# Kernel tuning notes

Measured on AMD Instinct MI355X. Metric: run time of the kernel, lower is better.

The kernel has to match this reference:

```python
import jax, jax.numpy as jnp
import numpy as np

NEG_SLOPE = 0.01  # nn.LeakyReLU default
N_NODES = 38332
POI_LEN = 38333
CAT_LEN = 400
POI_DIM = 300
CAT_DIM = 100
GCN_CH = 64
GCN_LAYERS = 5
N_EDGES = N_NODES * 32


def leaky(x):
    return jnp.where(x >= 0, x, NEG_SLOPE * x)


def gcn_conv(x, src, dst, W, b):
    """PyG GCNConv: add self loops + symmetric normalization.
    out = D^-1/2 (A+I) D^-1/2 X W + b, deg computed with self loops."""
    n = x.shape[0]
    h = x @ W  # [N, out]
    deg = jax.ops.segment_sum(jnp.ones_like(dst, dtype=h.dtype), dst, num_segments=n) + 1.0
    dinv = jax.lax.rsqrt(deg)  # deg >= 1 always (self loop)
    norm = dinv[src] * dinv[dst]  # [E]
    agg = jax.ops.segment_sum(h[src] * norm[:, None], dst, num_segments=n)
    agg = agg + h * (1.0 / deg)[:, None]  # self-loop term: norm_ii = 1/deg_i
    return agg + b


def setup_inputs() -> dict:
    key = jax.random.key(0)
    ks = jax.random.split(key, 16)
    poi_ids = jax.random.randint(ks[0], (N_NODES, 1), 0, POI_LEN).astype(jnp.float32)
    cat_ids = jax.random.randint(ks[1], (N_NODES, 1), 0, CAT_LEN).astype(jnp.float32)
    feats = jax.random.normal(ks[2], (N_NODES, 3), dtype=jnp.float32)
    x = jnp.concatenate([poi_ids, cat_ids, feats], axis=1)  # [N,5]
    edge_index = jax.random.randint(ks[3], (2, N_EDGES), 0, N_NODES, dtype=jnp.int32)

    def glorot(k, shape):
        lim = float(np.sqrt(6.0 / (shape[0] + shape[1])))
        return jax.random.uniform(k, shape, jnp.float32, -lim, lim)

    d_in = POI_DIM + CAT_DIM + 3  # 403
    params = {
        "poi_emb": jax.random.normal(ks[4], (POI_LEN, POI_DIM), jnp.float32),
        "cat_emb": jax.random.normal(ks[5], (CAT_LEN, CAT_DIM), jnp.float32),
        "W_in": glorot(ks[6], (d_in, GCN_CH)),
        "b_in": jnp.zeros((GCN_CH,), jnp.float32),
        "gcn_Ws": jnp.stack([glorot(jax.random.fold_in(ks[7], i), (GCN_CH, GCN_CH)) for i in range(GCN_LAYERS)]),
        "gcn_bs": jnp.zeros((GCN_LAYERS, GCN_CH), jnp.float32),
        "W_out": glorot(ks[8], (GCN_CH, 1)),
        "b_out": jnp.zeros((1,), jnp.float32),
        "fc1_W": glorot(ks[9], (N_NODES, 128)),
        "fc1_b": jnp.zeros((128,), jnp.float32),
        "fc2_W": glorot(ks[10], (128, POI_LEN)),
        "fc2_b": jnpos if False else jnp.zeros((POI_LEN,), jnp.float32),
    }
    return {"x": x, "edge_index": edge_index, **params}


def reference(x, edge_index, poi_emb, cat_emb, W_in, b_in, gcn_Ws, gcn_bs, W_out, b_out, fc1_W, fc1_b, fc2_W, fc2_b):
    src, dst = edge_index[0], edge_index[1]
    poi_f = poi_emb[x[:, 0].astype(jnp.int32)]  # [N,300]
    cat_f = cat_emb[x[:, 1].astype(jnp.int32)]  # [N,100]
    feat = jnp.concatenate([poi_f, cat_f, x[:, 2:5]], axis=1)  # [N,403]
    feat = leaky(gcn_conv(feat, src, dst, W_in, b_in))
    for i in range(GCN_LAYERS):
        t = gcn_conv(feat, src, dst, gcn_Ws[i], gcn_bs[i])
        feat = leaky(t) + t  # GcnUnit: relu(temp) + temp
    feat = leaky(gcn_conv(feat, src, dst, W_out, b_out)).reshape(-1)  # [N]
    h = jax.nn.relu(feat @ fc1_W + fc1_b)
    out = jax.nn.relu(h @ fc2_W + fc2_b)  # [poi_len]
    return out
```

## Files before the change

kernel.cpp:

```cpp
#include <hip/hip_runtime.h>
#include <hip/hip_bf16.h>

#define N_NODES 38332
#define POI_LEN 38333
#define CAT_LEN 400
#define POI_DIM 300
#define CAT_DIM 100
#define N_EDGES (N_NODES * 32)
#define NEG_SLOPE 0.01f
#define B1 ((N_NODES + 127) / 128)
#define SPLIT_CHUNK 2048
#define NSPLIT ((N_EDGES + SPLIT_CHUNK - 1) / SPLIT_CHUNK)
#define PLACE_CAP 8192
#define BCAP 8192

typedef __attribute__((ext_vector_type(8))) short short8;
typedef __attribute__((ext_vector_type(4))) float f32x4;

__device__ __forceinline__ unsigned short f2bf(float f) {
  unsigned u = __float_as_uint(f);
  u += 0x7fff + ((u >> 16) & 1);
  return (unsigned short)(u >> 16);
}
__device__ __forceinline__ float bflo(unsigned u) {
  return __uint_as_float(u << 16);
}
__device__ __forceinline__ float bfhi(unsigned u) {
  return __uint_as_float(u & 0xffff0000u);
}


#define WFIN_ELEMS (13 * 2048)
#define WFGCN_ELEMS (5 * 4096)

__global__ __launch_bounds__(256) void k_prep(const float* __restrict__ W_in,
                                              const float* __restrict__ gcn_Ws,
                                              unsigned short* __restrict__ wf_in,
                                              unsigned short* __restrict__ wf_gcn,
                                              int* __restrict__ bcnt,
                                              float* __restrict__ h128) {
  int idx = blockIdx.x * 256 + threadIdx.x;
  if (idx < B1) bcnt[idx] = 0;
  if (idx < 128) h128[idx] = 0.f;
  if (idx < WFIN_ELEMS) {
    int j = idx & 7, n = (idx >> 3) & 63, q = (idx >> 9) & 3, ks = idx >> 11;
    int k = ks * 32 + q * 8 + j;
    wf_in[idx] = f2bf((k < 400) ? W_in[k * 64 + n] : 0.f);
  } else if (idx < WFIN_ELEMS + WFGCN_ELEMS) {
    int t = idx - WFIN_ELEMS;
    int l = t >> 12, i = t & 4095;
    int j = i & 7, n = (i >> 3) & 63, q = (i >> 9) & 3, ks = i >> 11;
    int k = ks * 32 + q * 8 + j;
    wf_gcn[t] = f2bf(gcn_Ws[(size_t)l * 4096 + k * 64 + n]);
  }
}


__global__ __launch_bounds__(256) void k_split(const int* __restrict__ src,
                                               const int* __restrict__ dst,
                                               int* __restrict__ bcnt,
                                               int* __restrict__ staging) {
  __shared__ int hist[B1];
  __shared__ int lbase[B1];
  __shared__ int lcur[B1];
  int tid = threadIdx.x;
  int base = blockIdx.x * SPLIT_CHUNK;
  int n = N_EDGES - base;
  if (n > SPLIT_CHUNK) n = SPLIT_CHUNK;
  for (int b = tid; b < B1; b += 256) {
    hist[b] = 0;
    lcur[b] = 0;
  }
  __syncthreads();
  for (int i = tid; i < n; i += 256) atomicAdd(&hist[dst[base + i] >> 7], 1);
  __syncthreads();
  for (int b = tid; b < B1; b += 256) {
    int c = hist[b];
    lbase[b] = c ? atomicAdd(&bcnt[b], c) : 0;
  }
  __syncthreads();
  for (int i = tid; i < n; i += 256) {
    int d = dst[base + i];
    int s = src[base + i];
    int b = d >> 7;
    int off = atomicAdd(&lcur[b], 1);
    staging[(size_t)b * BCAP + lbase[b] + off] = (s << 7) | (d & 127);
  }
}

__global__ __launch_bounds__(256) void k_place(const int* __restrict__ staging,
                                               const int* __restrict__ bcnt,
                                               int* __restrict__ csr_src,
                                               int2* __restrict__ rs,
                                               float* __restrict__ dinv) {
  __shared__ int lc[128];
  __shared__ int ls[256];
  __shared__ int cur[128];
  __shared__ int buf[PLACE_CAP];
  int b = blockIdx.x;
  int tid = threadIdx.x;
  int d0 = b * 128;
  int nd = N_NODES - d0;
  if (nd > 128) nd = 128;
  int cnt_b = bcnt[b];
  const int* st = staging + (size_t)b * BCAP;
  if (tid < 128) lc[tid] = 0;
  __syncthreads();
  for (int i = tid; i < cnt_b; i += 256) atomicAdd(&lc[st[i] & 127], 1);
  __syncthreads();
  int v = (tid < 128) ? lc[tid] : 0;
  ls[tid] = v;
  __syncthreads();
  for (int off = 1; off < 128; off <<= 1) {
    int t = (tid >= off) ? ls[tid - off] : 0;
    __syncthreads();
    ls[tid] += t;
    __syncthreads();
  }
  if (tid < 128) {
    int excl = ls[tid] - v;
    cur[tid] = excl;
    if (tid < nd) {
      rs[d0 + tid] = make_int2(b * BCAP + excl, v);
      dinv[d0 + tid] = 1.0f / sqrtf((float)(v + 1));
    }
  }
  __syncthreads();
  for (int i = tid; i < cnt_b; i += 256) {
    int p = st[i];
    int pos = atomicAdd(&cur[p & 127], 1);
    buf[pos] = p >> 7;
  }
  __syncthreads();
  int base = b * BCAP;
  for (int i = tid; i < cnt_b; i += 256) csr_src[base + i] = buf[i];
}


__global__ __launch_bounds__(256) void k_front(
    const float* __restrict__ x, const float* __restrict__ poi_emb,
    const float* __restrict__ cat_emb, const float* __restrict__ W_in,
    const unsigned short* __restrict__ wf_in, const float* __restrict__ dinv,
    unsigned short* __restrict__ hs) {
  constexpr int KP = 416, RS = 424, NK4 = 104;
  __shared__ unsigned short sA[16 * RS];
  __shared__ float sC[16 * 68];
  __shared__ int sPid[16], sCid[16];
  __shared__ float sX[16][3];
  int tid = threadIdx.x;
  int row0 = blockIdx.x * 16;
  if (tid < 16) {
    int row = row0 + tid;
    if (row < N_NODES) {
      sPid[tid] = (int)x[row * 5 + 0];
      sCid[tid] = (int)x[row * 5 + 1];
      sX[tid][0] = x[row * 5 + 2];
      sX[tid][1] = x[row * 5 + 3];
      sX[tid][2] = x[row * 5 + 4];
    } else {
      sPid[tid] = 0; sCid[tid] = 0;
      sX[tid][0] = sX[tid][1] = sX[tid][2] = 0.f;
    }
  }
  __syncthreads();
  for (int idx = tid; idx < 16 * NK4; idx += 256) {
    int r = idx / NK4;
    int k = (idx - r * NK4) * 4;
    ushort4 o = {0, 0, 0, 0};
    if (k < 400 && row0 + r < N_NODES) {
      float4 f;
      if (k < 300) f = *(const float4*)(poi_emb + (size_t)sPid[r] * 300 + k);
      else         f = *(const float4*)(cat_emb + (size_t)sCid[r] * 100 + (k - 300));
      o.x = f2bf(f.x); o.y = f2bf(f.y); o.z = f2bf(f.z); o.w = f2bf(f.w);
    }
    *(ushort4*)&sA[r * RS + k] = o;
  }
  __syncthreads();
  int lane = tid & 63, wv = tid >> 6;
  int c = lane & 15, q = lane >> 4, n0 = wv * 16;
  f32x4 acc = {0.f, 0.f, 0.f, 0.f};
  const unsigned short* arow = &sA[c * RS];
#pragma unroll
  for (int ks = 0; ks < KP / 32; ks++) {
    short8 af = *(const short8*)(arow + ks * 32 + q * 8);
    short8 bf = *(const short8*)(wf_in + ((size_t)((ks * 4 + q) * 64 + n0 + c)) * 8);
    acc = __builtin_amdgcn_mfma_f32_16x16x32_bf16(af, bf, acc, 0, 0, 0);
  }
#pragma unroll
  for (int r = 0; r < 4; r++) sC[(q * 4 + r) * 68 + n0 + c] = acc[r];
  __syncthreads();
  for (int idx = tid; idx < 16 * 64; idx += 256) {
    int r = idx >> 6, col = idx & 63;
    int row = row0 + r;
    if (row < N_NODES) {
      float v = sC[r * 68 + col] + sX[r][0] * W_in[400 * 64 + col] +
                sX[r][1] * W_in[401 * 64 + col] + sX[r][2] * W_in[402 * 64 + col];
      hs[(size_t)row * 64 + col] = f2bf(v * dinv[row]);
    }
  }
}


template <int MODE>
__global__ __launch_bounds__(256) void k_agg(const unsigned short* __restrict__ hs,
                                             const int2* __restrict__ rs,
                                             const int* __restrict__ csr_src,
                                             const float* __restrict__ dinv,
                                             const float* __restrict__ bias,
                                             const unsigned short* __restrict__ Wf,
                                             unsigned short* __restrict__ hs_next,
                                             const float* __restrict__ W_out,
                                             float* __restrict__ hs1) {
  __shared__ unsigned short sA[16 * 72];
  __shared__ float sC[4 * 68];
  int tid = threadIdx.x;
  int lane = tid & 63;
  int wv = tid >> 6;
  int node = blockIdx.x * 4 + wv;
  int eslot = lane >> 3;
  int ch8 = lane & 7;
  if (MODE != 2) {
    for (int i = tid; i < 216; i += 256)
      *(ushort4*)&sA[288 + i * 4] = (ushort4){0, 0, 0, 0};
  }
  int2 rr = rs[node];
  int r0 = rr.x, r1 = rr.x + rr.y;
  float4 a0 = {0.f, 0.f, 0.f, 0.f}, a1 = a0;
#define ACC8(v)                                                              \
  do {                                                                       \
    a0.x += bflo((v).x); a0.y += bfhi((v).x);                                \
    a0.z += bflo((v).y); a0.w += bfhi((v).y);                                \
    a1.x += bflo((v).z); a1.y += bfhi((v).z);                                \
    a1.z += bflo((v).w); a1.w += bfhi((v).w);                                \
  } while (0)
  int e = r0 + eslot;
  for (; e + 24 < r1; e += 32) {
    int s0 = csr_src[e];
    int s1 = csr_src[e + 8];
    int s2 = csr_src[e + 16];
    int s3 = csr_src[e + 24];
    uint4 v0 = *(const uint4*)(hs + (size_t)s0 * 64 + ch8 * 8);
    uint4 v1 = *(const uint4*)(hs + (size_t)s1 * 64 + ch8 * 8);
    uint4 v2 = *(const uint4*)(hs + (size_t)s2 * 64 + ch8 * 8);
    uint4 v3 = *(const uint4*)(hs + (size_t)s3 * 64 + ch8 * 8);
    ACC8(v0); ACC8(v1); ACC8(v2); ACC8(v3);
  }
  if (e + 8 < r1) {
    int s0 = csr_src[e];
    int s1 = csr_src[e + 8];
    uint4 v0 = *(const uint4*)(hs + (size_t)s0 * 64 + ch8 * 8);
    uint4 v1 = *(const uint4*)(hs + (size_t)s1 * 64 + ch8 * 8);
    ACC8(v0); ACC8(v1);
    e += 16;
  }
  if (e < r1) {
    int s = csr_src[e];
    uint4 v = *(const uint4*)(hs + (size_t)s * 64 + ch8 * 8);
    ACC8(v);
  }
#undef ACC8
#pragma unroll
  for (int off = 8; off <= 32; off <<= 1) {
    a0.x += __shfl_xor(a0.x, off, 64);
    a0.y += __shfl_xor(a0.y, off, 64);
    a0.z += __shfl_xor(a0.z, off, 64);
    a0.w += __shfl_xor(a0.w, off, 64);
    a1.x += __shfl_xor(a1.x, off, 64);
    a1.y += __shfl_xor(a1.y, off, 64);
    a1.z += __shfl_xor(a1.z, off, 64);
    a1.w += __shfl_xor(a1.w, off, 64);
  }
  float dn = dinv[node];
  if (lane < 8) {
    uint4 sv = *(const uint4*)(hs + (size_t)node * 64 + ch8 * 8);
    float4 bb0 = *(const float4*)(bias + ch8 * 8);
    float4 bb1 = *(const float4*)(bias + ch8 * 8 + 4);
    float4 t0, t1;
    t0.x = dn * (a0.x + bflo(sv.x)) + bb0.x;
    t0.y = dn * (a0.y + bfhi(sv.x)) + bb0.y;
    t0.z = dn * (a0.z + bflo(sv.y)) + bb0.z;
    t0.w = dn * (a0.w + bfhi(sv.y)) + bb0.w;
    t1.x = dn * (a1.x + bflo(sv.z)) + bb1.x;
    t1.y = dn * (a1.y + bfhi(sv.z)) + bb1.y;
    t1.z = dn * (a1.z + bflo(sv.w)) + bb1.z;
    t1.w = dn * (a1.w + bfhi(sv.w)) + bb1.w;
    float4 l0, l1, o0, o1;
    l0.x = (t0.x >= 0.f) ? t0.x : NEG_SLOPE * t0.x;
    l0.y = (t0.y >= 0.f) ? t0.y : NEG_SLOPE * t0.y;
    l0.z = (t0.z >= 0.f) ? t0.z : NEG_SLOPE * t0.z;
    l0.w = (t0.w >= 0.f) ? t0.w : NEG_SLOPE * t0.w;
    l1.x = (t1.x >= 0.f) ? t1.x : NEG_SLOPE * t1.x;
    l1.y = (t1.y >= 0.f) ? t1.y : NEG_SLOPE * t1.y;
    l1.z = (t1.z >= 0.f) ? t1.z : NEG_SLOPE * t1.z;
    l1.w = (t1.w >= 0.f) ? t1.w : NEG_SLOPE * t1.w;
    if (MODE == 0) {
      o0 = l0; o1 = l1;
    } else {
      o0.x = l0.x + t0.x; o0.y = l0.y + t0.y; o0.z = l0.z + t0.z; o0.w = l0.w + t0.w;
      o1.x = l1.x + t1.x; o1.y = l1.y + t1.y; o1.z = l1.z + t1.z; o1.w = l1.w + t1.w;
    }
    if (MODE == 2) {
      float4 w0 = *(const float4*)(W_out + ch8 * 8);
      float4 w1 = *(const float4*)(W_out + ch8 * 8 + 4);
      float p = o0.x * w0.x + o0.y * w0.y + o0.z * w0.z + o0.w * w0.w +
                o1.x * w1.x + o1.y * w1.y + o1.z * w1.z + o1.w * w1.w;
      p += __shfl_xor(p, 1, 64);
      p += __shfl_xor(p, 2, 64);
      p += __shfl_xor(p, 4, 64);
      if (lane == 0) hs1[node] = p * dn;
    } else {
      uint4 pk;
      pk.x = (unsigned)f2bf(o0.x) | ((unsigned)f2bf(o0.y) << 16);
      pk.y = (unsigned)f2bf(o0.z) | ((unsigned)f2bf(o0.w) << 16);
      pk.z = (unsigned)f2bf(o1.x) | ((unsigned)f2bf(o1.y) << 16);
      pk.w = (unsigned)f2bf(o1.z) | ((unsigned)f2bf(o1.w) << 16);
      *(uint4*)&sA[wv * 72 + ch8 * 8] = pk;
    }
  }
  if (MODE != 2) {
    __syncthreads();
    int c = lane & 15, q = lane >> 4, n0 = wv * 16;
    f32x4 acc = {0.f, 0.f, 0.f, 0.f};
    const unsigned short* arow = &sA[c * 72];
#pragma unroll
    for (int ks = 0; ks < 2; ks++) {
      short8 af = *(const short8*)(arow + ks * 32 + q * 8);
      short8 bf = *(const short8*)(Wf + ((size_t)((ks * 4 + q) * 64 + n0 + c)) * 8);
      acc = __builtin_amdgcn_mfma_f32_16x16x32_bf16(af, bf, acc, 0, 0, 0);
    }
    if (q == 0) {
#pragma unroll
      for (int r = 0; r < 4; r++) sC[r * 68 + n0 + c] = acc[r];
    }
    __syncthreads();
    if (tid < 128) {
      int r = tid >> 5, c2 = (tid & 31) * 2;
      int row = blockIdx.x * 4 + r;
      float dr = dinv[row];
      unsigned lo = f2bf(sC[r * 68 + c2] * dr);
      unsigned hi = f2bf(sC[r * 68 + c2 + 1] * dr);
      *(unsigned*)(hs_next + (size_t)row * 64 + c2) = lo | (hi << 16);
    }
  }
}


__global__ __launch_bounds__(256) void k_out_agg(const float* __restrict__ hs1,
                                                 const int2* __restrict__ rs,
                                                 const int* __restrict__ csr_src,
                                                 const float* __restrict__ dinv,
                                                 const float* __restrict__ b_out,
                                                 float* __restrict__ g) {
  int lane = threadIdx.x & 63;
  int w = threadIdx.x >> 6;
  int node = blockIdx.x * 4 + w;
  int2 rr = rs[node];
  int r0 = rr.x, r1 = rr.x + rr.y;
  float acc = 0.f;
  for (int e = r0 + lane; e < r1; e += 64) acc += hs1[csr_src[e]];
#pragma unroll
  for (int off = 32; off; off >>= 1) acc += __shfl_xor(acc, off, 64);
  if (lane == 0) {
    float t = dinv[node] * (acc + hs1[node]) + b_out[0];
    g[node] = (t >= 0.f) ? t : NEG_SLOPE * t;
  }
}


__global__ __launch_bounds__(128) void k_fc1(const float* __restrict__ g,
                                             const float* __restrict__ fc1_W,
                                             float* __restrict__ h128) {
  int j = threadIdx.x;
  int base = blockIdx.x * 32;
  int end = base + 32;
  if (end > N_NODES) end = N_NODES;
  float acc = 0.f;
  int i = base;
  for (; i + 4 <= end; i += 4) {
    acc += g[i + 0] * fc1_W[(size_t)(i + 0) * 128 + j];
    acc += g[i + 1] * fc1_W[(size_t)(i + 1) * 128 + j];
    acc += g[i + 2] * fc1_W[(size_t)(i + 2) * 128 + j];
    acc += g[i + 3] * fc1_W[(size_t)(i + 3) * 128 + j];
  }
  for (; i < end; i++) acc += g[i] * fc1_W[(size_t)i * 128 + j];
  atomicAdd(&h128[j], acc);
}

__global__ __launch_bounds__(256) void k_fc2(const float* __restrict__ h128raw,
                                             const float* __restrict__ fc1_b,
                                             const float* __restrict__ fc2_W,
                                             const float* __restrict__ fc2_b,
                                             float* __restrict__ out) {
  __shared__ float sh[128];
  int tid = threadIdx.x;
  if (tid < 128) {
    float v = h128raw[tid] + fc1_b[tid];
    sh[tid] = (v > 0.f) ? v : 0.f;
  }
  __syncthreads();
  int p = blockIdx.x * 256 + tid;
  if (p < POI_LEN) {
    float acc = fc2_b[p];
#pragma unroll 8
    for (int j = 0; j < 128; j++) acc += sh[j] * fc2_W[(size_t)j * POI_LEN + p];
    out[p] = (acc > 0.f) ? acc : 0.f;
  }
}


extern "C" void kernel_launch(void* const* d_in, const int* in_sizes, int n_in,
                              void* d_out, int out_size, void* d_ws, size_t ws_size,
                              hipStream_t stream) {
  const float* x       = (const float*)d_in[0];
  const int*   ei      = (const int*)d_in[1];
  const float* poi_emb = (const float*)d_in[2];
  const float* cat_emb = (const float*)d_in[3];
  const float* W_in    = (const float*)d_in[4];
  const float* b_in    = (const float*)d_in[5];
  const float* gcn_Ws  = (const float*)d_in[6];
  const float* gcn_bs  = (const float*)d_in[7];
  const float* W_out   = (const float*)d_in[8];
  const float* b_out   = (const float*)d_in[9];
  const float* fc1_W   = (const float*)d_in[10];
  const float* fc1_b   = (const float*)d_in[11];
  const float* fc2_W   = (const float*)d_in[12];
  const float* fc2_b   = (const float*)d_in[13];
  const int* src = ei;
  const int* dst = ei + N_EDGES;

  char* p = (char*)d_ws;
  auto take = [&](size_t bytes) {
    char* r = p;
    p += (bytes + 255) & ~(size_t)255;
    return r;
  };
  int2*  rs        = (int2*)take((size_t)N_NODES * 8);
  float* dinv      = (float*)take((size_t)N_NODES * 4);
  int*   bcnt      = (int*)take((size_t)B1 * 4);
  int*   csr_src   = (int*)take((size_t)B1 * BCAP * 4);
  unsigned short* hsA = (unsigned short*)take((size_t)N_NODES * 64 * 2);
  unsigned short* hsB = (unsigned short*)take((size_t)N_NODES * 64 * 2);
  float* hs1       = (float*)take((size_t)N_NODES * 4);
  float* g         = (float*)take((size_t)N_NODES * 4);
  float* h128      = (float*)take(128 * 4);
  unsigned short* wf_in  = (unsigned short*)take((size_t)WFIN_ELEMS * 2);
  unsigned short* wf_gcn = (unsigned short*)take((size_t)WFGCN_ELEMS * 2);
  int* staging = (int*)hsA;
  float* out = (float*)d_out;

  const int nb4 = N_NODES / 4;
  const int nb16 = (N_NODES + 15) / 16;

  k_prep<<<(WFIN_ELEMS + WFGCN_ELEMS + 255) / 256, 256, 0, stream>>>(
      W_in, gcn_Ws, wf_in, wf_gcn, bcnt, h128);
  k_split<<<NSPLIT, 256, 0, stream>>>(src, dst, bcnt, staging);
  k_place<<<B1, 256, 0, stream>>>(staging, bcnt, csr_src, rs, dinv);

  k_front<<<nb16, 256, 0, stream>>>(x, poi_emb, cat_emb, W_in, wf_in, dinv, hsA);

  k_agg<0><<<nb4, 256, 0, stream>>>(hsA, rs, csr_src, dinv, b_in,
                                    wf_gcn + 0 * 4096, hsB, nullptr, nullptr);
  k_agg<1><<<nb4, 256, 0, stream>>>(hsB, rs, csr_src, dinv, gcn_bs + 0 * 64,
                                    wf_gcn + 1 * 4096, hsA, nullptr, nullptr);
  k_agg<1><<<nb4, 256, 0, stream>>>(hsA, rs, csr_src, dinv, gcn_bs + 1 * 64,
                                    wf_gcn + 2 * 4096, hsB, nullptr, nullptr);
  k_agg<1><<<nb4, 256, 0, stream>>>(hsB, rs, csr_src, dinv, gcn_bs + 2 * 64,
                                    wf_gcn + 3 * 4096, hsA, nullptr, nullptr);
  k_agg<1><<<nb4, 256, 0, stream>>>(hsA, rs, csr_src, dinv, gcn_bs + 3 * 64,
                                    wf_gcn + 4 * 4096, hsB, nullptr, nullptr);
  k_agg<2><<<nb4, 256, 0, stream>>>(hsB, rs, csr_src, dinv, gcn_bs + 4 * 64,
                                    nullptr, nullptr, W_out, hs1);

  k_out_agg<<<nb4, 256, 0, stream>>>(hs1, rs, csr_src, dinv, b_out, g);
  k_fc1<<<(N_NODES + 31) / 32, 128, 0, stream>>>(g, fc1_W, h128);
  k_fc2<<<(POI_LEN + 255) / 256, 256, 0, stream>>>(h128, fc1_b, fc2_W, fc2_b, out);
}
```

Before: 408.2 us.

## Fuse place, front, GCN layers and FC stages into one cooperative persistent kernel

Replaces the chain of separate kernels (CSR placement, front projection, six aggregation layers, output aggregation, fc1, fc2) with a single cooperative kernel that runs persistent blocks and uses grid-wide syncs between phases. Aggregation now handles two nodes per wavefront with eight edge slots unrolled, and fc2 splits the reduction across four warps per block. The aim is to remove launch gaps and tail effects between the many small kernels. In exchange it adds grid-sync costs and limits occupancy to what fits co-resident, with large shared memory per block.

```diff
diff --git a/kernel.cpp b/kernel.cpp
--- a/kernel.cpp
+++ b/kernel.cpp
@@ -1,5 +1,8 @@
 #include <hip/hip_runtime.h>
 #include <hip/hip_bf16.h>
+#include <hip/hip_cooperative_groups.h>
+
+namespace cg = cooperative_groups;
 
 #define N_NODES 38332
 #define POI_LEN 38333
@@ -11,7 +14,6 @@
 #define B1 ((N_NODES + 127) / 128)
 #define SPLIT_CHUNK 2048
 #define NSPLIT ((N_EDGES + SPLIT_CHUNK - 1) / SPLIT_CHUNK)
-#define PLACE_CAP 8192
 #define BCAP 8192
 
 typedef __attribute__((ext_vector_type(8))) short short8;
@@ -27,6 +29,10 @@
 }
 __device__ __forceinline__ float bfhi(unsigned u) {
   return __uint_as_float(u & 0xffff0000u);
+}
+__device__ __forceinline__ void acc8(float4& a0, float4& a1, uint4 v) {
+  a0.x += bflo(v.x); a0.y += bfhi(v.x); a0.z += bflo(v.y); a0.w += bfhi(v.y);
+  a1.x += bflo(v.z); a1.y += bfhi(v.z); a1.z += bflo(v.w); a1.w += bfhi(v.w);
 }
 
 
@@ -88,329 +94,371 @@
   }
 }
 
-__global__ __launch_bounds__(256) void k_place(const int* __restrict__ staging,
-                                               const int* __restrict__ bcnt,
-                                               int* __restrict__ csr_src,
-                                               int2* __restrict__ rs,
-                                               float* __restrict__ dinv) {
-  __shared__ int lc[128];
-  __shared__ int ls[256];
-  __shared__ int cur[128];
-  __shared__ int buf[PLACE_CAP];
-  int b = blockIdx.x;
-  int tid = threadIdx.x;
-  int d0 = b * 128;
-  int nd = N_NODES - d0;
-  if (nd > 128) nd = 128;
-  int cnt_b = bcnt[b];
-  const int* st = staging + (size_t)b * BCAP;
-  if (tid < 128) lc[tid] = 0;
-  __syncthreads();
-  for (int i = tid; i < cnt_b; i += 256) atomicAdd(&lc[st[i] & 127], 1);
-  __syncthreads();
-  int v = (tid < 128) ? lc[tid] : 0;
-  ls[tid] = v;
-  __syncthreads();
-  for (int off = 1; off < 128; off <<= 1) {
-    int t = (tid >= off) ? ls[tid - off] : 0;
-    __syncthreads();
-    ls[tid] += t;
-    __syncthreads();
-  }
-  if (tid < 128) {
-    int excl = ls[tid] - v;
-    cur[tid] = excl;
-    if (tid < nd) {
-      rs[d0 + tid] = make_int2(b * BCAP + excl, v);
-      dinv[d0 + tid] = 1.0f / sqrtf((float)(v + 1));
-    }
-  }
-  __syncthreads();
-  for (int i = tid; i < cnt_b; i += 256) {
-    int p = st[i];
-    int pos = atomicAdd(&cur[p & 127], 1);
-    buf[pos] = p >> 7;
-  }
-  __syncthreads();
-  int base = b * BCAP;
-  for (int i = tid; i < cnt_b; i += 256) csr_src[base + i] = buf[i];
-}
-
-
-__global__ __launch_bounds__(256) void k_front(
-    const float* __restrict__ x, const float* __restrict__ poi_emb,
-    const float* __restrict__ cat_emb, const float* __restrict__ W_in,
-    const unsigned short* __restrict__ wf_in, const float* __restrict__ dinv,
-    unsigned short* __restrict__ hs) {
-  constexpr int KP = 416, RS = 424, NK4 = 104;
-  __shared__ unsigned short sA[16 * RS];
-  __shared__ float sC[16 * 68];
-  __shared__ int sPid[16], sCid[16];
-  __shared__ float sX[16][3];
-  int tid = threadIdx.x;
-  int row0 = blockIdx.x * 16;
-  if (tid < 16) {
-    int row = row0 + tid;
-    if (row < N_NODES) {
-      sPid[tid] = (int)x[row * 5 + 0];
-      sCid[tid] = (int)x[row * 5 + 1];
-      sX[tid][0] = x[row * 5 + 2];
-      sX[tid][1] = x[row * 5 + 3];
-      sX[tid][2] = x[row * 5 + 4];
-    } else {
-      sPid[tid] = 0; sCid[tid] = 0;
-      sX[tid][0] = sX[tid][1] = sX[tid][2] = 0.f;
-    }
-  }
-  __syncthreads();
-  for (int idx = tid; idx < 16 * NK4; idx += 256) {
-    int r = idx / NK4;
-    int k = (idx - r * NK4) * 4;
-    ushort4 o = {0, 0, 0, 0};
-    if (k < 400 && row0 + r < N_NODES) {
-      float4 f;
-      if (k < 300) f = *(const float4*)(poi_emb + (size_t)sPid[r] * 300 + k);
-      else         f = *(const float4*)(cat_emb + (size_t)sCid[r] * 100 + (k - 300));
-      o.x = f2bf(f.x); o.y = f2bf(f.y); o.z = f2bf(f.z); o.w = f2bf(f.w);
-    }
-    *(ushort4*)&sA[r * RS + k] = o;
-  }
-  __syncthreads();
-  int lane = tid & 63, wv = tid >> 6;
-  int c = lane & 15, q = lane >> 4, n0 = wv * 16;
-  f32x4 acc = {0.f, 0.f, 0.f, 0.f};
-  const unsigned short* arow = &sA[c * RS];
-#pragma unroll
-  for (int ks = 0; ks < KP / 32; ks++) {
-    short8 af = *(const short8*)(arow + ks * 32 + q * 8);
-    short8 bf = *(const short8*)(wf_in + ((size_t)((ks * 4 + q) * 64 + n0 + c)) * 8);
-    acc = __builtin_amdgcn_mfma_f32_16x16x32_bf16(af, bf, acc, 0, 0, 0);
-  }
-#pragma unroll
-  for (int r = 0; r < 4; r++) sC[(q * 4 + r) * 68 + n0 + c] = acc[r];
-  __syncthreads();
-  for (int idx = tid; idx < 16 * 64; idx += 256) {
-    int r = idx >> 6, col = idx & 63;
-    int row = row0 + r;
-    if (row < N_NODES) {
-      float v = sC[r * 68 + col] + sX[r][0] * W_in[400 * 64 + col] +
-                sX[r][1] * W_in[401 * 64 + col] + sX[r][2] * W_in[402 * 64 + col];
-      hs[(size_t)row * 64 + col] = f2bf(v * dinv[row]);
-    }
-  }
-}
-
-
-template <int MODE>
-__global__ __launch_bounds__(256) void k_agg(const unsigned short* __restrict__ hs,
-                                             const int2* __restrict__ rs,
-                                             const int* __restrict__ csr_src,
-                                             const float* __restrict__ dinv,
-                                             const float* __restrict__ bias,
-                                             const unsigned short* __restrict__ Wf,
-                                             unsigned short* __restrict__ hs_next,
-                                             const float* __restrict__ W_out,
-                                             float* __restrict__ hs1) {
-  __shared__ unsigned short sA[16 * 72];
-  __shared__ float sC[4 * 68];
+
+struct MegaParams {
+  const float* x;
+  const float* poi_emb;
+  const float* cat_emb;
+  const float* W_in;
+  const float* b_in;
+  const float* gcn_bs;
+  const float* W_out;
+  const float* b_out;
+  const float* fc1_W;
+  const float* fc1_b;
+  const float* fc2_W;
+  const float* fc2_b;
+  const int* staging;
+  const int* bcnt;
+  int* csr_src;
+  int2* rs;
+  float* dinv;
+  const unsigned short* wf_in;
+  const unsigned short* wf_gcn;
+  unsigned short* hsA;
+  unsigned short* hsB;
+  float* hs1;
+  float* g;
+  float* h128;
+  float* out;
+};
+
+__device__ __forceinline__ void agg_phase(
+    int mode, const unsigned short* __restrict__ hin,
+    unsigned short* __restrict__ hout, const unsigned short* __restrict__ Wf,
+    const float* __restrict__ bias, const int2* __restrict__ rs,
+    const int* __restrict__ csr, const float* __restrict__ dinv,
+    const float* __restrict__ W_out, float* __restrict__ hs1, char* SM,
+    int nb) {
+  unsigned short* sA = (unsigned short*)SM;
+  float* sC = (float*)(SM + 2304);
   int tid = threadIdx.x;
   int lane = tid & 63;
   int wv = tid >> 6;
-  int node = blockIdx.x * 4 + wv;
-  int eslot = lane >> 3;
+  int hseg = lane >> 5;
+  int es = (lane >> 3) & 3;
   int ch8 = lane & 7;
-  if (MODE != 2) {
-    for (int i = tid; i < 216; i += 256)
-      *(ushort4*)&sA[288 + i * 4] = (ushort4){0, 0, 0, 0};
-  }
-  int2 rr = rs[node];
-  int r0 = rr.x, r1 = rr.x + rr.y;
-  float4 a0 = {0.f, 0.f, 0.f, 0.f}, a1 = a0;
-#define ACC8(v)                                                              \
-  do {                                                                       \
-    a0.x += bflo((v).x); a0.y += bfhi((v).x);                                \
-    a0.z += bflo((v).y); a0.w += bfhi((v).y);                                \
-    a1.x += bflo((v).z); a1.y += bfhi((v).z);                                \
-    a1.z += bflo((v).w); a1.w += bfhi((v).w);                                \
-  } while (0)
-  int e = r0 + eslot;
-  for (; e + 24 < r1; e += 32) {
-    int s0 = csr_src[e];
-    int s1 = csr_src[e + 8];
-    int s2 = csr_src[e + 16];
-    int s3 = csr_src[e + 24];
-    uint4 v0 = *(const uint4*)(hs + (size_t)s0 * 64 + ch8 * 8);
-    uint4 v1 = *(const uint4*)(hs + (size_t)s1 * 64 + ch8 * 8);
-    uint4 v2 = *(const uint4*)(hs + (size_t)s2 * 64 + ch8 * 8);
-    uint4 v3 = *(const uint4*)(hs + (size_t)s3 * 64 + ch8 * 8);
-    ACC8(v0); ACC8(v1); ACC8(v2); ACC8(v3);
-  }
-  if (e + 8 < r1) {
-    int s0 = csr_src[e];
-    int s1 = csr_src[e + 8];
-    uint4 v0 = *(const uint4*)(hs + (size_t)s0 * 64 + ch8 * 8);
-    uint4 v1 = *(const uint4*)(hs + (size_t)s1 * 64 + ch8 * 8);
-    ACC8(v0); ACC8(v1);
-    e += 16;
-  }
-  if (e < r1) {
-    int s = csr_src[e];
-    uint4 v = *(const uint4*)(hs + (size_t)s * 64 + ch8 * 8);
-    ACC8(v);
-  }
-#undef ACC8
+  if (mode != 2) {
+    for (int i = tid; i < 72; i += 256)
+      *(ushort4*)(SM + 1152 + i * 8) = (ushort4){0, 0, 0, 0};
+  }
+  for (int grp = blockIdx.x; grp < (N_NODES + 7) / 8; grp += nb) {
+    int node = grp * 8 + wv * 2 + hseg;
+    bool valid = node < N_NODES;
+    int2 rr = valid ? rs[node] : make_int2(0, 0);
+    int r0 = rr.x, r1 = rr.x + rr.y;
+    float dn = valid ? dinv[node] : 0.f;
+    uint4 sv = {0, 0, 0, 0};
+    if (valid && (lane & 31) < 8)
+      sv = *(const uint4*)(hin + (size_t)node * 64 + ch8 * 8);
+    float4 a0 = {0.f, 0.f, 0.f, 0.f}, a1 = a0;
+    int e = r0 + es;
+    for (; e + 28 < r1; e += 32) {
+      int s0 = csr[e], s1 = csr[e + 4], s2 = csr[e + 8], s3 = csr[e + 12];
+      int s4 = csr[e + 16], s5 = csr[e + 20], s6 = csr[e + 24], s7 = csr[e + 28];
+      uint4 v0 = *(const uint4*)(hin + (size_t)s0 * 64 + ch8 * 8);
+      uint4 v1 = *(const uint4*)(hin + (size_t)s1 * 64 + ch8 * 8);
+      uint4 v2 = *(const uint4*)(hin + (size_t)s2 * 64 + ch8 * 8);
+      uint4 v3 = *(const uint4*)(hin + (size_t)s3 * 64 + ch8 * 8);
+      uint4 v4 = *(const uint4*)(hin + (size_t)s4 * 64 + ch8 * 8);
+      uint4 v5 = *(const uint4*)(hin + (size_t)s5 * 64 + ch8 * 8);
+      uint4 v6 = *(const uint4*)(hin + (size_t)s6 * 64 + ch8 * 8);
+      uint4 v7 = *(const uint4*)(hin + (size_t)s7 * 64 + ch8 * 8);
+      acc8(a0, a1, v0); acc8(a0, a1, v1); acc8(a0, a1, v2); acc8(a0, a1, v3);
+      acc8(a0, a1, v4); acc8(a0, a1, v5); acc8(a0, a1, v6); acc8(a0, a1, v7);
+    }
+    for (; e + 4 < r1; e += 8) {
+      int s0 = csr[e], s1 = csr[e + 4];
+      uint4 v0 = *(const uint4*)(hin + (size_t)s0 * 64 + ch8 * 8);
+      uint4 v1 = *(const uint4*)(hin + (size_t)s1 * 64 + ch8 * 8);
+      acc8(a0, a1, v0); acc8(a0, a1, v1);
+    }
+    if (e < r1) {
+      int s0 = csr[e];
+      uint4 v0 = *(const uint4*)(hin + (size_t)s0 * 64 + ch8 * 8);
+      acc8(a0, a1, v0);
+    }
 #pragma unroll
-  for (int off = 8; off <= 32; off <<= 1) {
-    a0.x += __shfl_xor(a0.x, off, 64);
-    a0.y += __shfl_xor(a0.y, off, 64);
-    a0.z += __shfl_xor(a0.z, off, 64);
-    a0.w += __shfl_xor(a0.w, off, 64);
-    a1.x += __shfl_xor(a1.x, off, 64);
-    a1.y += __shfl_xor(a1.y, off, 64);
-    a1.z += __shfl_xor(a1.z, off, 64);
-    a1.w += __shfl_xor(a1.w, off, 64);
-  }
-  float dn = dinv[node];
-  if (lane < 8) {
-    uint4 sv = *(const uint4*)(hs + (size_t)node * 64 + ch8 * 8);
-    float4 bb0 = *(const float4*)(bias + ch8 * 8);
-    float4 bb1 = *(const float4*)(bias + ch8 * 8 + 4);
-    float4 t0, t1;
-    t0.x = dn * (a0.x + bflo(sv.x)) + bb0.x;
-    t0.y = dn * (a0.y + bfhi(sv.x)) + bb0.y;
-    t0.z = dn * (a0.z + bflo(sv.y)) + bb0.z;
-    t0.w = dn * (a0.w + bfhi(sv.y)) + bb0.w;
-    t1.x = dn * (a1.x + bflo(sv.z)) + bb1.x;
-    t1.y = dn * (a1.y + bfhi(sv.z)) + bb1.y;
-    t1.z = dn * (a1.z + bflo(sv.w)) + bb1.z;
-    t1.w = dn * (a1.w + bfhi(sv.w)) + bb1.w;
-    float4 l0, l1, o0, o1;
-    l0.x = (t0.x >= 0.f) ? t0.x : NEG_SLOPE * t0.x;
-    l0.y = (t0.y >= 0.f) ? t0.y : NEG_SLOPE * t0.y;
-    l0.z = (t0.z >= 0.f) ? t0.z : NEG_SLOPE * t0.z;
-    l0.w = (t0.w >= 0.f) ? t0.w : NEG_SLOPE * t0.w;
-    l1.x = (t1.x >= 0.f) ? t1.x : NEG_SLOPE * t1.x;
-    l1.y = (t1.y >= 0.f) ? t1.y : NEG_SLOPE * t1.y;
-    l1.z = (t1.z >= 0.f) ? t1.z : NEG_SLOPE * t1.z;
-    l1.w = (t1.w >= 0.f) ? t1.w : NEG_SLOPE * t1.w;
-    if (MODE == 0) {
-      o0 = l0; o1 = l1;
-    } else {
-      o0.x = l0.x + t0.x; o0.y = l0.y + t0.y; o0.z = l0.z + t0.z; o0.w = l0.w + t0.w;
-      o1.x = l1.x + t1.x; o1.y = l1.y + t1.y; o1.z = l1.z + t1.z; o1.w = l1.w + t1.w;
-    }
-    if (MODE == 2) {
-      float4 w0 = *(const float4*)(W_out + ch8 * 8);
-      float4 w1 = *(const float4*)(W_out + ch8 * 8 + 4);
-      float p = o0.x * w0.x + o0.y * w0.y + o0.z * w0.z + o0.w * w0.w +
-                o1.x * w1.x + o1.y * w1.y + o1.z * w1.z + o1.w * w1.w;
-      p += __shfl_xor(p, 1, 64);
-      p += __shfl_xor(p, 2, 64);
-      p += __shfl_xor(p, 4, 64);
-      if (lane == 0) hs1[node] = p * dn;
-    } else {
-      uint4 pk;
-      pk.x = (unsigned)f2bf(o0.x) | ((unsigned)f2bf(o0.y) << 16);
-      pk.y = (unsigned)f2bf(o0.z) | ((unsigned)f2bf(o0.w) << 16);
-      pk.z = (unsigned)f2bf(o1.x) | ((unsigned)f2bf(o1.y) << 16);
-      pk.w = (unsigned)f2bf(o1.z) | ((unsigned)f2bf(o1.w) << 16);
-      *(uint4*)&sA[wv * 72 + ch8 * 8] = pk;
-    }
-  }
-  if (MODE != 2) {
+    for (int off = 8; off <= 16; off <<= 1) {
+      a0.x += __shfl_xor(a0.x, off, 64); a0.y += __shfl_xor(a0.y, off, 64);
+      a0.z += __shfl_xor(a0.z, off, 64); a0.w += __shfl_xor(a0.w, off, 64);
+      a1.x += __shfl_xor(a1.x, off, 64); a1.y += __shfl_xor(a1.y, off, 64);
+      a1.z += __shfl_xor(a1.z, off, 64); a1.w += __shfl_xor(a1.w, off, 64);
+    }
+    if ((lane & 31) < 8) {
+      float4 bb0 = *(const float4*)(bias + ch8 * 8);
+      float4 bb1 = *(const float4*)(bias + ch8 * 8 + 4);
+      float4 t0, t1;
+      t0.x = dn * (a0.x + bflo(sv.x)) + bb0.x;
+      t0.y = dn * (a0.y + bfhi(sv.x)) + bb0.y;
+      t0.z = dn * (a0.z + bflo(sv.y)) + bb0.z;
+      t0.w = dn * (a0.w + bfhi(sv.y)) + bb0.w;
+      t1.x = dn * (a1.x + bflo(sv.z)) + bb1.x;
+      t1.y = dn * (a1.y + bfhi(sv.z)) + bb1.y;
+      t1.z = dn * (a1.z + bflo(sv.w)) + bb1.z;
+      t1.w = dn * (a1.w + bfhi(sv.w)) + bb1.w;
+      float4 l0, l1, o0, o1;
+      l0.x = (t0.x >= 0.f) ? t0.x : NEG_SLOPE * t0.x;
+      l0.y = (t0.y >= 0.f) ? t0.y : NEG_SLOPE * t0.y;
+      l0.z = (t0.z >= 0.f) ? t0.z : NEG_SLOPE * t0.z;
+      l0.w = (t0.w >= 0.f) ? t0.w : NEG_SLOPE * t0.w;
+      l1.x = (t1.x >= 0.f) ? t1.x : NEG_SLOPE * t1.x;
+      l1.y = (t1.y >= 0.f) ? t1.y : NEG_SLOPE * t1.y;
+      l1.z = (t1.z >= 0.f) ? t1.z : NEG_SLOPE * t1.z;
+      l1.w = (t1.w >= 0.f) ? t1.w : NEG_SLOPE * t1.w;
+      if (mode == 0) {
+        o0 = l0; o1 = l1;
+      } else {
+        o0.x = l0.x + t0.x; o0.y = l0.y + t0.y;
+        o0.z = l0.z + t0.z; o0.w = l0.w + t0.w;
+        o1.x = l1.x + t1.x; o1.y = l1.y + t1.y;
+        o1.z = l1.z + t1.z; o1.w = l1.w + t1.w;
+      }
+      if (mode == 2) {
+        float4 w0 = *(const float4*)(W_out + ch8 * 8);
+        float4 w1 = *(const float4*)(W_out + ch8 * 8 + 4);
+        float p = o0.x * w0.x + o0.y * w0.y + o0.z * w0.z + o0.w * w0.w +
+                  o1.x * w1.x + o1.y * w1.y + o1.z * w1.z + o1.w * w1.w;
+        p += __shfl_xor(p, 1, 64);
+        p += __shfl_xor(p, 2, 64);
+        p += __shfl_xor(p, 4, 64);
+        if ((lane & 31) == 0 && valid) hs1[node] = p * dn;
+      } else if (valid) {
+        uint4 pk;
+        pk.x = (unsigned)f2bf(o0.x) | ((unsigned)f2bf(o0.y) << 16);
+        pk.y = (unsigned)f2bf(o0.z) | ((unsigned)f2bf(o0.w) << 16);
+        pk.z = (unsigned)f2bf(o1.x) | ((unsigned)f2bf(o1.y) << 16);
+        pk.w = (unsigned)f2bf(o1.z) | ((unsigned)f2bf(o1.w) << 16);
+        *(uint4*)&sA[(wv * 2 + hseg) * 72 + ch8 * 8] = pk;
+      }
+    }
+    if (mode != 2) {
+      __syncthreads();
+      int c = lane & 15, q = lane >> 4, n0 = wv * 16;
+      f32x4 acc = {0.f, 0.f, 0.f, 0.f};
+      const unsigned short* arow = &sA[c * 72];
+#pragma unroll
+      for (int ks = 0; ks < 2; ks++) {
+        short8 af = *(const short8*)(arow + ks * 32 + q * 8);
+        short8 bf =
+            *(const short8*)(Wf + ((size_t)((ks * 4 + q) * 64 + n0 + c)) * 8);
+        acc = __builtin_amdgcn_mfma_f32_16x16x32_bf16(af, bf, acc, 0, 0, 0);
+      }
+      if (q < 2) {
+#pragma unroll
+        for (int r = 0; r < 4; r++) sC[(q * 4 + r) * 68 + n0 + c] = acc[r];
+      }
+      __syncthreads();
+      for (int idx = tid; idx < 8 * 64; idx += 256) {
+        int r = idx >> 6, col = idx & 63;
+        int n2 = grp * 8 + r;
+        if (n2 < N_NODES)
+          hout[(size_t)n2 * 64 + col] = f2bf(sC[r * 68 + col] * dinv[n2]);
+      }
+    }
+  }
+}
+
+__global__ __launch_bounds__(256, 4) void k_mega(MegaParams P) {
+  cg::grid_group grid = cg::this_grid();
+  __shared__ __align__(16) char SM[34816];
+  int tid = threadIdx.x;
+  int nb = gridDim.x;
+
+  {
+    int* lc = (int*)SM;
+    int* ls = lc + 128;
+    int* cur = ls + 256;
+    int* buf = cur + 128;
+    for (int b = blockIdx.x; b < B1; b += nb) {
+      int d0 = b * 128;
+      int nd = N_NODES - d0;
+      if (nd > 128) nd = 128;
+      int cnt_b = P.bcnt[b];
+      const int* st = P.staging + (size_t)b * BCAP;
+      if (tid < 128) lc[tid] = 0;
+      __syncthreads();
+      for (int i = tid; i < cnt_b; i += 256) atomicAdd(&lc[st[i] & 127], 1);
+      __syncthreads();
+      int v = (tid < 128) ? lc[tid] : 0;
+      ls[tid] = v;
+      __syncthreads();
+      for (int off = 1; off < 128; off <<= 1) {
+        int t = (tid >= off) ? ls[tid - off] : 0;
+        __syncthreads();
+        ls[tid] += t;
+        __syncthreads();
+      }
+      if (tid < 128) {
+        int excl = ls[tid] - v;
+        cur[tid] = excl;
+        if (tid < nd) {
+          P.rs[d0 + tid] = make_int2(b * BCAP + excl, v);
+          P.dinv[d0 + tid] = 1.0f / sqrtf((float)(v + 1));
+        }
+      }
+      __syncthreads();
+      for (int i = tid; i < cnt_b; i += 256) {
+        int pk = st[i];
+        int pos = atomicAdd(&cur[pk & 127], 1);
+        buf[pos] = pk >> 7;
+      }
+      __syncthreads();
+      int base = b * BCAP;
+      for (int i = tid; i < cnt_b; i += 256) P.csr_src[base + i] = buf[i];
+      __syncthreads();
+    }
+  }
+  grid.sync();
+
+  {
+    unsigned short* sA = (unsigned short*)SM;
+    float* sC = (float*)(SM + 13568);
+    int* sPid = (int*)(SM + 17920);
+    int* sCid = (int*)(SM + 17984);
+    float* sX = (float*)(SM + 18048);
+    int lane = tid & 63, wv = tid >> 6;
+    for (int t0 = blockIdx.x; t0 < (N_NODES + 15) / 16; t0 += nb) {
+      int row0 = t0 * 16;
+      if (tid < 16) {
+        int row = row0 + tid;
+        if (row < N_NODES) {
+          sPid[tid] = (int)P.x[row * 5 + 0];
+          sCid[tid] = (int)P.x[row * 5 + 1];
+          sX[tid * 3 + 0] = P.x[row * 5 + 2];
+          sX[tid * 3 + 1] = P.x[row * 5 + 3];
+          sX[tid * 3 + 2] = P.x[row * 5 + 4];
+        } else {
+          sPid[tid] = 0;
+          sCid[tid] = 0;
+          sX[tid * 3 + 0] = sX[tid * 3 + 1] = sX[tid * 3 + 2] = 0.f;
+        }
+      }
+      __syncthreads();
+      for (int idx = tid; idx < 16 * 104; idx += 256) {
+        int r = idx / 104;
+        int k = (idx - r * 104) * 4;
+        ushort4 o = {0, 0, 0, 0};
+        if (k < 400 && row0 + r < N_NODES) {
+          float4 f;
+          if (k < 300)
+            f = *(const float4*)(P.poi_emb + (size_t)sPid[r] * 300 + k);
+          else
+            f = *(const float4*)(P.cat_emb + (size_t)sCid[r] * 100 + (k - 300));
+          o.x = f2bf(f.x); o.y = f2bf(f.y); o.z = f2bf(f.z); o.w = f2bf(f.w);
+        }
+        *(ushort4*)&sA[r * 424 + k] = o;
+      }
+      __syncthreads();
+      int c = lane & 15, q = lane >> 4, n0 = wv * 16;
+      f32x4 acc = {0.f, 0.f, 0.f, 0.f};
+      const unsigned short* arow = &sA[c * 424];
+#pragma unroll
+      for (int ks = 0; ks < 13; ks++) {
+        short8 af = *(const short8*)(arow + ks * 32 + q * 8);
+        short8 bf = *(const short8*)(P.wf_in +
+                                     ((size_t)((ks * 4 + q) * 64 + n0 + c)) * 8);
+        acc = __builtin_amdgcn_mfma_f32_16x16x32_bf16(af, bf, acc, 0, 0, 0);
+      }
+#pragma unroll
+      for (int r = 0; r < 4; r++) sC[(q * 4 + r) * 68 + n0 + c] = acc[r];
+      __syncthreads();
+      for (int idx = tid; idx < 16 * 64; idx += 256) {
+        int r = idx >> 6, col = idx & 63;
+        int row = row0 + r;
+        if (row < N_NODES) {
+          float v = sC[r * 68 + col] + sX[r * 3 + 0] * P.W_in[400 * 64 + col] +
+                    sX[r * 3 + 1] * P.W_in[401 * 64 + col] +
+                    sX[r * 3 + 2] * P.W_in[402 * 64 + col];
+          P.hsA[(size_t)row * 64 + col] = f2bf(v * P.dinv[row]);
+        }
+      }
+      __syncthreads();
+    }
+  }
+  grid.sync();
+
+  for (int l = 0; l < 5; l++) {
+    const unsigned short* hin = (l & 1) ? P.hsB : P.hsA;
+    unsigned short* hout = (l & 1) ? P.hsA : P.hsB;
+    const float* bias = (l == 0) ? P.b_in : (P.gcn_bs + (size_t)(l - 1) * 64);
+    agg_phase(l == 0 ? 0 : 1, hin, hout, P.wf_gcn + (size_t)l * 4096, bias,
+              P.rs, P.csr_src, P.dinv, nullptr, nullptr, SM, nb);
+    grid.sync();
+  }
+  agg_phase(2, P.hsB, nullptr, nullptr, P.gcn_bs + 4 * 64, P.rs, P.csr_src,
+            P.dinv, P.W_out, P.hs1, SM, nb);
+  grid.sync();
+
+  {
+    int lane = tid & 63, wv = tid >> 6;
+    for (int grp = blockIdx.x; grp < (N_NODES + 3) / 4; grp += nb) {
+      int node = grp * 4 + wv;
+      int2 rr = P.rs[node];
+      int r0 = rr.x, r1 = rr.x + rr.y;
+      float acc = 0.f;
+      for (int e = r0 + lane; e < r1; e += 64) acc += P.hs1[P.csr_src[e]];
+#pragma unroll
+      for (int off = 32; off; off >>= 1) acc += __shfl_xor(acc, off, 64);
+      if (lane == 0) {
+        float t = P.dinv[node] * (acc + P.hs1[node]) + P.b_out[0];
+        P.g[node] = (t >= 0.f) ? t : NEG_SLOPE * t;
+      }
+    }
+  }
+  grid.sync();
+
+  {
+    int j = tid & 127, half = tid >> 7;
+    for (int c = blockIdx.x; c < 599; c += nb) {
+      int i0 = c * 64 + half * 32;
+      int i1 = i0 + 32;
+      if (i1 > N_NODES) i1 = N_NODES;
+      float acc = 0.f;
+      for (int i = i0; i < i1; i++)
+        acc += P.g[i] * P.fc1_W[(size_t)i * 128 + j];
+      atomicAdd(&P.h128[j], acc);
+    }
+  }
+  grid.sync();
+
+  {
+    float* sh = (float*)SM;
+    float* red = sh + 128;
+    if (tid < 128) {
+      float v = P.h128[tid] + P.fc1_b[tid];
+      sh[tid] = (v > 0.f) ? v : 0.f;
+    }
     __syncthreads();
-    int c = lane & 15, q = lane >> 4, n0 = wv * 16;
-    f32x4 acc = {0.f, 0.f, 0.f, 0.f};
-    const unsigned short* arow = &sA[c * 72];
-#pragma unroll
-    for (int ks = 0; ks < 2; ks++) {
-      short8 af = *(const short8*)(arow + ks * 32 + q * 8);
-      short8 bf = *(const short8*)(Wf + ((size_t)((ks * 4 + q) * 64 + n0 + c)) * 8);
-      acc = __builtin_amdgcn_mfma_f32_16x16x32_bf16(af, bf, acc, 0, 0, 0);
-    }
-    if (q == 0) {
-#pragma unroll
-      for (int r = 0; r < 4; r++) sC[r * 68 + n0 + c] = acc[r];
-    }
-    __syncthreads();
-    if (tid < 128) {
-      int r = tid >> 5, c2 = (tid & 31) * 2;
-      int row = blockIdx.x * 4 + r;
-      float dr = dinv[row];
-      unsigned lo = f2bf(sC[r * 68 + c2] * dr);
-      unsigned hi = f2bf(sC[r * 68 + c2 + 1] * dr);
-      *(unsigned*)(hs_next + (size_t)row * 64 + c2) = lo | (hi << 16);
-    }
-  }
-}
-
-
-__global__ __launch_bounds__(256) void k_out_agg(const float* __restrict__ hs1,
-                                                 const int2* __restrict__ rs,
-                                                 const int* __restrict__ csr_src,
-                                                 const float* __restrict__ dinv,
-                                                 const float* __restrict__ b_out,
-                                                 float* __restrict__ g) {
-  int lane = threadIdx.x & 63;
-  int w = threadIdx.x >> 6;
-  int node = blockIdx.x * 4 + w;
-  int2 rr = rs[node];
-  int r0 = rr.x, r1 = rr.x + rr.y;
-  float acc = 0.f;
-  for (int e = r0 + lane; e < r1; e += 64) acc += hs1[csr_src[e]];
-#pragma unroll
-  for (int off = 32; off; off >>= 1) acc += __shfl_xor(acc, off, 64);
-  if (lane == 0) {
-    float t = dinv[node] * (acc + hs1[node]) + b_out[0];
-    g[node] = (t >= 0.f) ? t : NEG_SLOPE * t;
-  }
-}
-
-
-__global__ __launch_bounds__(128) void k_fc1(const float* __restrict__ g,
-                                             const float* __restrict__ fc1_W,
-                                             float* __restrict__ h128) {
-  int j = threadIdx.x;
-  int base = blockIdx.x * 32;
-  int end = base + 32;
-  if (end > N_NODES) end = N_NODES;
-  float acc = 0.f;
-  int i = base;
-  for (; i + 4 <= end; i += 4) {
-    acc += g[i + 0] * fc1_W[(size_t)(i + 0) * 128 + j];
-    acc += g[i + 1] * fc1_W[(size_t)(i + 1) * 128 + j];
-    acc += g[i + 2] * fc1_W[(size_t)(i + 2) * 128 + j];
-    acc += g[i + 3] * fc1_W[(size_t)(i + 3) * 128 + j];
-  }
-  for (; i < end; i++) acc += g[i] * fc1_W[(size_t)i * 128 + j];
-  atomicAdd(&h128[j], acc);
-}
-
-__global__ __launch_bounds__(256) void k_fc2(const float* __restrict__ h128raw,
-                                             const float* __restrict__ fc1_b,
-                                             const float* __restrict__ fc2_W,
-                                             const float* __restrict__ fc2_b,
-                                             float* __restrict__ out) {
-  __shared__ float sh[128];
-  int tid = threadIdx.x;
-  if (tid < 128) {
-    float v = h128raw[tid] + fc1_b[tid];
-    sh[tid] = (v > 0.f) ? v : 0.f;
-  }
-  __syncthreads();
-  int p = blockIdx.x * 256 + tid;
-  if (p < POI_LEN) {
-    float acc = fc2_b[p];
+    int pl = tid & 63, jg = tid >> 6;
+    for (int c = blockIdx.x; c < 599; c += nb) {
+      int p = c * 64 + pl;
+      float acc = 0.f;
+      if (p < POI_LEN) {
+        const float* wp = P.fc2_W + (size_t)(jg * 32) * POI_LEN + p;
 #pragma unroll 8
-    for (int j = 0; j < 128; j++) acc += sh[j] * fc2_W[(size_t)j * POI_LEN + p];
-    out[p] = (acc > 0.f) ? acc : 0.f;
+        for (int jj = 0; jj < 32; jj++)
+          acc += sh[jg * 32 + jj] * wp[(size_t)jj * POI_LEN];
+      }
+      red[jg * 64 + pl] = acc;
+      __syncthreads();
+      if (tid < 64) {
+        int pp = c * 64 + tid;
+        if (pp < POI_LEN) {
+          float v = P.fc2_b[pp] + red[tid] + red[64 + tid] + red[128 + tid] +
+                    red[192 + tid];
+          P.out[pp] = (v > 0.f) ? v : 0.f;
+        }
+      }
+      __syncthreads();
+    }
   }
 }
 
 
 extern "C" void kernel_launch(void* const* d_in, const int* in_sizes, int n_in,
-                              void* d_out, int out_size, void* d_ws, size_t ws_size,
-                              hipStream_t stream) {
+                              void* d_out, int out_size, void* d_ws,
+                              size_t ws_size, hipStream_t stream) {
   const float* x       = (const float*)d_in[0];
   const int*   ei      = (const int*)d_in[1];
   const float* poi_emb = (const float*)d_in[2];
@@ -434,44 +482,46 @@
     p += (bytes + 255) & ~(size_t)255;
     return r;
   };
-  int2*  rs        = (int2*)take((size_t)N_NODES * 8);
-  float* dinv      = (float*)take((size_t)N_NODES * 4);
-  int*   bcnt      = (int*)take((size_t)B1 * 4);
-  int*   csr_src   = (int*)take((size_t)B1 * BCAP * 4);
+  int2*  rs      = (int2*)take((size_t)N_NODES * 8);
+  float* dinv    = (float*)take((size_t)N_NODES * 4);
+  int*   bcnt    = (int*)take((size_t)B1 * 4);
+  int*   csr_src = (int*)take((size_t)B1 * BCAP * 4);
   unsigned short* hsA = (unsigned short*)take((size_t)N_NODES * 64 * 2);
   unsigned short* hsB = (unsigned short*)take((size_t)N_NODES * 64 * 2);
-  float* hs1       = (float*)take((size_t)N_NODES * 4);
-  float* g         = (float*)take((size_t)N_NODES * 4);
-  float* h128      = (float*)take(128 * 4);
+  float* hs1     = (float*)take((size_t)N_NODES * 4);
+  float* g       = (float*)take((size_t)N_NODES * 4);
+  float* h128    = (float*)take(128 * 4);
   unsigned short* wf_in  = (unsigned short*)take((size_t)WFIN_ELEMS * 2);
   unsigned short* wf_gcn = (unsigned short*)take((size_t)WFGCN_ELEMS * 2);
   int* staging = (int*)hsA;
   float* out = (float*)d_out;
 
-  const int nb4 = N_NODES / 4;
-  const int nb16 = (N_NODES + 15) / 16;
-
-  k_prep<<<(WFIN_ELEMS + WFGCN_ELEMS + 255) / 256, 256, 0, stream>>>(
+  k_prep<<<(WFIN_ELEMS + WFGCN_ELEMS + 255) / 256 + 1, 256, 0, stream>>>(
       W_in, gcn_Ws, wf_in, wf_gcn, bcnt, h128);
   k_split<<<NSPLIT, 256, 0, stream>>>(src, dst, bcnt, staging);
-  k_place<<<B1, 256, 0, stream>>>(staging, bcnt, csr_src, rs, dinv);
-
-  k_front<<<nb16, 256, 0, stream>>>(x, poi_emb, cat_emb, W_in, wf_in, dinv, hsA);
-
-  k_agg<0><<<nb4, 256, 0, stream>>>(hsA, rs, csr_src, dinv, b_in,
-                                    wf_gcn + 0 * 4096, hsB, nullptr, nullptr);
-  k_agg<1><<<nb4, 256, 0, stream>>>(hsB, rs, csr_src, dinv, gcn_bs + 0 * 64,
-                                    wf_gcn + 1 * 4096, hsA, nullptr, nullptr);
-  k_agg<1><<<nb4, 256, 0, stream>>>(hsA, rs, csr_src, dinv, gcn_bs + 1 * 64,
-                                    wf_gcn + 2 * 4096, hsB, nullptr, nullptr);
-  k_agg<1><<<nb4, 256, 0, stream>>>(hsB, rs, csr_src, dinv, gcn_bs + 2 * 64,
-                                    wf_gcn + 3 * 4096, hsA, nullptr, nullptr);
-  k_agg<1><<<nb4, 256, 0, stream>>>(hsA, rs, csr_src, dinv, gcn_bs + 3 * 64,
-                                    wf_gcn + 4 * 4096, hsB, nullptr, nullptr);
-  k_agg<2><<<nb4, 256, 0, stream>>>(hsB, rs, csr_src, dinv, gcn_bs + 4 * 64,
-                                    nullptr, nullptr, W_out, hs1);
-
-  k_out_agg<<<nb4, 256, 0, stream>>>(hs1, rs, csr_src, dinv, b_out, g);
-  k_fc1<<<(N_NODES + 31) / 32, 128, 0, stream>>>(g, fc1_W, h128);
-  k_fc2<<<(POI_LEN + 255) / 256, 256, 0, stream>>>(h128, fc1_b, fc2_W, fc2_b, out);
-}
+
+  MegaParams P;
+  P.x = x; P.poi_emb = poi_emb; P.cat_emb = cat_emb;
+  P.W_in = W_in; P.b_in = b_in; P.gcn_bs = gcn_bs;
+  P.W_out = W_out; P.b_out = b_out;
+  P.fc1_W = fc1_W; P.fc1_b = fc1_b; P.fc2_W = fc2_W; P.fc2_b = fc2_b;
+  P.staging = staging; P.bcnt = bcnt;
+  P.csr_src = csr_src; P.rs = rs; P.dinv = dinv;
+  P.wf_in = wf_in; P.wf_gcn = wf_gcn;
+  P.hsA = hsA; P.hsB = hsB;
+  P.hs1 = hs1; P.g = g; P.h128 = h128; P.out = out;
+
+  static int g_nb = 0;
+  if (g_nb == 0) {
+    int maxb = 0;
+    hipOccupancyMaxActiveBlocksPerMultiprocessor(&maxb, k_mega, 256, 0);
+    if (maxb < 1) maxb = 1;
+    if (maxb > 8) maxb = 8;
+    int cus = 0;
+    hipDeviceGetAttribute(&cus, hipDeviceAttributeMultiprocessorCount, 0);
+    if (cus <= 0) cus = 256;
+    g_nb = maxb * cus;
+  }
+  void* args[] = {(void*)&P};
+  hipLaunchCooperativeKernel(k_mega, dim3(g_nb), dim3(256), args, 0, stream);
+}
```

Result: slower. 1.125 ms (+175.6%).
